# Performance work log

Measured on AMD Instinct MI355X. Metric: run time of the kernel, lower is better.

The kernel has to match this reference:

```python
import jax, jax.numpy as jnp
import numpy as np

PSEUDO3D = True
DO_TUBE = True
DILATION_ITERATIONS = 1

# Neighbor offsets P2..P9 (clockwise from north), as in Zhang-Suen / skimage skeletonize
_OFFS = [(-1, 0), (-1, 1), (0, 1), (1, 1), (1, 0), (1, -1), (0, -1), (-1, -1)]


def _shift(a, dy, dx):
    # out[n, y, x] = a[n, y+dy, x+dx], zero-padded borders (same as skimage's 0-pad)
    N, H, W = a.shape
    p = jnp.pad(a, ((0, 0), (1, 1), (1, 1)))
    return p[:, 1 + dy:1 + dy + H, 1 + dx:1 + dx + W]


def _subiter(img, first):
    # One Zhang-Suen sub-iteration on a stack of 2D slices [N, H, W] (bool)
    P = [_shift(img, dy, dx) for dy, dx in _OFFS]
    B = sum(p.astype(jnp.int32) for p in P)            # nonzero-neighbor count
    seq = P + [P[0]]
    A = sum(((~seq[k]) & seq[k + 1]).astype(jnp.int32) for k in range(8))  # 0->1 transitions
    P2, P3, P4, P5, P6, P7, P8, P9 = P
    if first:
        c = (~(P2 & P4 & P6)) & (~(P4 & P6 & P8))
    else:
        c = (~(P2 & P4 & P8)) & (~(P2 & P6 & P8))
    remove = img & (B >= 2) & (B <= 6) & (A == 1) & c
    return img & ~remove


def _thin_stack(stack):
    # Zhang-Suen thinning of every 2D slice in a [N, H, W] bool stack, run to convergence.
    # All slices are processed in one while_loop; converged slices are fixed points, so
    # extra iterations are no-ops and the result matches per-slice skeletonize.
    def body(state):
        img, _ = state
        new = _subiter(_subiter(img, True), False)
        return new, jnp.any(new != img)

    def cond(state):
        return state[1]

    img, _ = jax.lax.while_loop(cond, body, (stack, jnp.array(True)))
    return img


def _dilate6(v):
    # scipy.ndimage.binary_dilation with the default 6-connected 3D structure, border 0
    D, H, W = v.shape
    p = jnp.pad(v, 1)
    out = v
    for dz, dy, dx in [(1, 0, 0), (-1, 0, 0), (0, 1, 0), (0, -1, 0), (0, 0, 1), (0, 0, -1)]:
        out = out | p[1 + dz:1 + dz + D, 1 + dy:1 + dy + H, 1 + dx:1 + dx + W]
    return out


def setup_inputs() -> dict:
    key = jax.random.key(0)
    gt = jax.random.randint(key, (1, 48, 384, 384), 0, 2).astype(jnp.float32)
    return {"gt_skel": gt}


def reference(gt_skel):
    vol = gt_skel[0]                      # squeeze(axis=0) -> [D, H, W]
    mask = vol == 1.0                     # bool
    skel = _thin_stack(mask)              # per z-slice skeletonize
    if PSEUDO3D:
        # per y-slice: mask[:, y, :] has shape [D, W]
        skel = skel | jnp.transpose(_thin_stack(jnp.transpose(mask, (1, 0, 2))), (1, 0, 2))
        # per x-slice: mask[:, :, x] has shape [D, H]
        skel = skel | jnp.transpose(_thin_stack(jnp.transpose(mask, (2, 0, 1))), (1, 2, 0))
    if DO_TUBE:
        for _ in range(DILATION_ITERATIONS):
            skel = _dilate6(skel)
    skel = skel & mask                    # skel &= gt_skel.astype(bool) (values are 0/1)
    return skel[None].astype(jnp.float32)
```

## Files before the change

kernel.cpp:

```cpp
#include <hip/hip_runtime.h>

typedef unsigned long long u64;

constexpr int D = 48, H = 384, W = 384;
constexpr int WPR = 6;
constexpr int PADW = 8;
constexpr int NVOX = D * H * W;
constexpr int NWVOL = D * H * WPR;
constexpr int MPAD2 = 52;
constexpr int NXY = (D + 2) * PADW;
constexpr int NTILE = D * 36;

constexpr int BAND = 96;
constexpr int HALO = 16;
constexpr int KA = 16;
constexpr int BROWS = BAND + 2 * HALO;
constexpr int NBAND = H / BAND;

__device__ __forceinline__ void fa(u64 a, u64 b, u64 c, u64& s, u64& cy) {
  u64 x = a ^ b;
  s = x ^ c;
  cy = (a & b) | (c & x);
}

__device__ __forceinline__ u64 zs_regs(u64 w00, u64 w01, u64 w02,
                                       u64 w10, u64 w11, u64 w12,
                                       u64 w20, u64 w21, u64 w22, bool first) {
  const u64 P2 = w01;
  const u64 P3 = (w01 >> 1) | (w02 << 63);
  const u64 P4 = (w11 >> 1) | (w12 << 63);
  const u64 P5 = (w21 >> 1) | (w22 << 63);
  const u64 P6 = w21;
  const u64 P7 = (w21 << 1) | (w20 >> 63);
  const u64 P8 = (w11 << 1) | (w10 >> 63);
  const u64 P9 = (w01 << 1) | (w00 >> 63);

  u64 s1, c1, s2, c2, s3, c3, u0, u1, v1, v2;
  fa(P2, P3, P4, s1, c1);
  fa(P5, P6, P7, s2, c2);
  fa(P8, P9, 0ull, s3, c3);
  fa(s1, s2, s3, u0, u1);
  fa(c1, c2, c3, v1, v2);
  u64 b1 = u1 ^ v1, k2 = u1 & v1;
  u64 b2 = v2 ^ k2, b3 = v2 & k2;
  u64 condB = (b1 | b2 | b3) & ~(b3 | (b2 & b1 & u0));

  u64 t0 = ~P2 & P3, t1 = ~P3 & P4, t2 = ~P4 & P5, t3 = ~P5 & P6;
  u64 t4 = ~P6 & P7, t5 = ~P7 & P8, t6 = ~P8 & P9, t7 = ~P9 & P2;
  fa(t0, t1, t2, s1, c1);
  fa(t3, t4, t5, s2, c2);
  fa(t6, t7, 0ull, s3, c3);
  fa(s1, s2, s3, u0, u1);
  fa(c1, c2, c3, v1, v2);
  u64 a1 = u1 ^ v1, j2 = u1 & v1;
  u64 a2 = v2 ^ j2, a3 = v2 & j2;
  u64 condA = u0 & ~(a1 | a2 | a3);

  u64 cc = first ? ((~(P2 & P4 & P6)) & (~(P4 & P6 & P8)))
                 : ((~(P2 & P4 & P8)) & (~(P2 & P6 & P8)));
  return w11 & ~(condB & condA & cc);
}

__device__ __forceinline__ u64 dirty_wave(const u64* __restrict__ U, int mw) {
  const u64 A = U[mw - 1], B = U[mw], C = U[mw + 1], Dw = U[mw + 2];
  const u64 smA = A | (A >> 1 | B << 63) | (A >> 2 | B << 62);
  const u64 smB = B | (B >> 1 | C << 63) | (B >> 2 | C << 62);
  const u64 smC = C | (C >> 1 | Dw << 63) | (C >> 2 | Dw << 62);
  const u64 Dm9 = (smB << 9) | (smA >> 55);
  const u64 Dm1 = (smB << 1) | (smA >> 63);
  const u64 Dp7 = (smB >> 7) | (smC << 57);
  return Dm9 | Dm1 | Dp7;
}

template<int R, bool FIRST>
__device__ __forceinline__ void subpass(const u64* __restrict__ src, u64* __restrict__ dst,
                                        u64* rawW, const u64* rawPrev,
                                        u64* Uw, const u64* Ur,
                                        int* chgflag, int tid) {
  constexpr int NP = (R + 2) * PADW;
  int anych = 0;
  for (int base = 0; base < NP; base += 1024) {
    const int idx = base + tid;
    int changed = 0;
    if (idx < NP) {
      const int mw = 1 + (idx >> 6);
      const u64 dmask = dirty_wave(Ur, mw);
      if ((dmask >> (idx & 63)) & 1ull) {
        const u64 old = src[idx];
        u64 nw = 0;
        if (old) {
          nw = zs_regs(src[idx - PADW - 1], src[idx - PADW], src[idx - PADW + 1],
                       src[idx - 1], old, src[idx + 1],
                       src[idx + PADW - 1], src[idx + PADW], src[idx + PADW + 1], FIRST);
          changed = (nw != old);
        }
        dst[idx] = nw;
        anych |= changed;
      }
    }
    const u64 bal = __ballot(changed != 0);
    if ((tid & 63) == 0 && idx < NP) {
      const int mw = 1 + (idx >> 6);
      rawW[mw] = bal;
      Uw[mw] = bal | rawPrev[mw];
    }
  }
  if (anych) *chgflag = 1;
}

template<int MW>
__device__ __forceinline__ void init_masks(u64 (*raw)[MPAD2], u64 (*Um)[MPAD2], int tid) {
  for (int t = tid; t < 4 * MPAD2; t += 1024) {
    const int arr = t / MPAD2, j = t - arr * MPAD2;
    const u64 v = ((arr & 1) && j >= 1 && j <= MW) ? ~0ull : 0ull;
    if (arr < 2) raw[arr][j] = v; else Um[arr - 2][j] = v;
  }
}

template<bool FIRST>
__device__ __forceinline__ void xy_dense(const u64* __restrict__ src, u64* __restrict__ dst,
                                         int* chgflag, int tid) {
  int anych = 0;
  if (tid < NXY) {
    const u64 old = src[tid];
    u64 nw = 0;
    if (old) {
      nw = zs_regs(src[tid - PADW - 1], src[tid - PADW], src[tid - PADW + 1],
                   src[tid - 1], old, src[tid + 1],
                   src[tid + PADW - 1], src[tid + PADW], src[tid + PADW + 1], FIRST);
      anych = (nw != old);
    }
    dst[tid] = nw;
  }
  if (anych) *chgflag = 1;
}

__device__ __forceinline__ void band_body(const u64* __restrict__ maskP,
                                          u64* __restrict__ curZ,
                                          int zi, int band, u64* Abuf, u64* Bbuf,
                                          u64 (*raw)[MPAD2], u64 (*Um)[MPAD2],
                                          int* s_chg) {
  constexpr int NP = (BROWS + 2) * PADW;
  constexpr int MW = (NP + 63) >> 6;
  const int tid = threadIdx.x;
  const int g0 = band * BAND - HALO;

  for (int idx = tid; idx < NP; idx += 1024) {
    const int rp = idx >> 3, cp = idx & 7;
    const int g = g0 + rp - 1;
    u64 v = 0;
    if (rp >= 1 && rp <= BROWS && cp >= 1 && cp <= 6 && g >= 0 && g < H)
      v = maskP[(zi * H + g) * WPR + (cp - 1)];
    Abuf[idx] = v;
    Bbuf[idx] = 0;
  }
  init_masks<MW>(raw, Um, tid);
  if (tid == 0) s_chg[0] = 0;
  __syncthreads();

  for (int t = 0; t < KA; t += 2) {
    subpass<BROWS, true >(Abuf, Bbuf, raw[0], raw[1], Um[0], Um[1], &s_chg[0], tid);
    __syncthreads();
    subpass<BROWS, false>(Bbuf, Abuf, raw[1], raw[0], Um[1], Um[0], &s_chg[0], tid);
    __syncthreads();
  }

  for (int idx = tid; idx < NP; idx += 1024) {
    const int rp = idx >> 3, cp = idx & 7;
    if (rp < 1 || rp > BROWS || cp < 1 || cp > 6) continue;
    const int g = g0 + rp - 1;
    if (g < band * BAND || g >= band * BAND + BAND) continue;
    curZ[(zi * H + g) * WPR + (cp - 1)] = Abuf[idx];
  }
}

template<int MODE>
__device__ __forceinline__ void thin_xy(const u64* __restrict__ maskP,
                                        u64* __restrict__ dstBuf,
                                        int slice, u64* Abuf, u64* Bbuf,
                                        int* s_chg) {
  const int tid = threadIdx.x;

  if (MODE == 1) {
    if (tid < NXY) {
      const int rp = tid >> 3, cp = tid & 7;
      u64 v = 0;
      if (rp >= 1 && rp <= D && cp >= 1 && cp <= 6)
        v = maskP[((rp - 1) * H + slice) * WPR + (cp - 1)];
      Abuf[tid] = v;
      Bbuf[tid] = 0;
    }
  } else {
    const int lane = tid & 63, wave = tid >> 6;
    const int xw = slice >> 6, xb = slice & 63;
    for (int w = wave; w < NXY; w += 16) {
      const int rp = w >> 3, cp = w & 7;
      u64 val = 0;
      if (rp >= 1 && rp <= D && cp >= 1 && cp <= 6) {
        const int c = (cp - 1) * 64 + lane;
        u64 bit = (maskP[((rp - 1) * H + c) * WPR + xw] >> xb) & 1ull;
        val = __ballot(bit != 0);
      }
      if (lane == 0) { Abuf[w] = val; Bbuf[w] = 0; }
    }
  }
  if (tid < 2) s_chg[tid] = 0;
  __syncthreads();

  int k = 0;
  while (true) {
    xy_dense<true >(Abuf, Bbuf, &s_chg[k], tid);
    __syncthreads();
    if (tid == 0) s_chg[k ^ 1] = 0;
    xy_dense<false>(Bbuf, Abuf, &s_chg[k], tid);
    __syncthreads();
    if (s_chg[k] == 0) break;
    k ^= 1;
  }

  if (tid < NXY) {
    const int rp = tid >> 3, cp = tid & 7;
    if (rp >= 1 && rp <= D && cp >= 1 && cp <= 6) {
      const u64 w = Abuf[tid];
      if (MODE == 1) dstBuf[((rp - 1) * H + slice) * WPR + (cp - 1)] = w;
      else           dstBuf[((rp - 1) * W + slice) * WPR + (cp - 1)] = w;
    }
  }
}

__global__ __launch_bounds__(1024) void thin_bands_xy(const u64* __restrict__ maskP,
                                                      u64* __restrict__ skelY,
                                                      u64* __restrict__ skelX,
                                                      u64* __restrict__ curZ) {
  __shared__ u64 Abuf[(BROWS + 2) * PADW];
  __shared__ u64 Bbuf[(BROWS + 2) * PADW];
  __shared__ u64 raw[2][MPAD2];
  __shared__ u64 Um[2][MPAD2];
  __shared__ int s_chg[2];
  const int b = blockIdx.x;
  if (b < D * NBAND) {
    band_body(maskP, curZ, b >> 2, b & 3, Abuf, Bbuf, raw, Um, s_chg);
  } else {
    const int q = b - D * NBAND;
    if (q < H) thin_xy<1>(maskP, skelY, q, Abuf, Bbuf, s_chg);
    else       thin_xy<2>(maskP, skelX, q - H, Abuf, Bbuf, s_chg);
  }
}

__global__ __launch_bounds__(1024) void thin_z_finish(const u64* __restrict__ curZ,
                                                      u64* __restrict__ skelZ,
                                                      const u64* __restrict__ skelX,
                                                      u64* __restrict__ skelXT) {
  __shared__ u64 Abuf[(H + 2) * PADW];
  __shared__ u64 Bbuf[(H + 2) * PADW];
  __shared__ u64 raw[2][MPAD2];
  __shared__ u64 Um[2][MPAD2];
  __shared__ int s_chg[2];
  const int b = blockIdx.x;
  const int tid = threadIdx.x;

  if (b < D) {
    constexpr int NP = (H + 2) * PADW;
    constexpr int MW = (NP + 63) >> 6;
    for (int idx = tid; idx < NP; idx += 1024) {
      const int rp = idx >> 3, cp = idx & 7;
      u64 v = 0;
      if (rp >= 1 && rp <= H && cp >= 1 && cp <= 6)
        v = curZ[(b * H + (rp - 1)) * WPR + (cp - 1)];
      Abuf[idx] = v;
      Bbuf[idx] = 0;
    }
    init_masks<MW>(raw, Um, tid);
    if (tid < 2) s_chg[tid] = 0;
    __syncthreads();

    int k = 0;
    while (true) {
      subpass<H, true >(Abuf, Bbuf, raw[0], raw[1], Um[0], Um[1], &s_chg[k], tid);
      __syncthreads();
      if (tid == 0) s_chg[k ^ 1] = 0;
      subpass<H, false>(Bbuf, Abuf, raw[1], raw[0], Um[1], Um[0], &s_chg[k], tid);
      __syncthreads();
      if (s_chg[k] == 0) break;
      k ^= 1;
    }

    for (int idx = tid; idx < NP; idx += 1024) {
      const int rp = idx >> 3, cp = idx & 7;
      if (rp < 1 || rp > H || cp < 1 || cp > 6) continue;
      skelZ[(b * H + (rp - 1)) * WPR + (cp - 1)] = Abuf[idx];
    }
  } else {
    const int gw = (b - D) * 16 + (tid >> 6);
    if (gw < NTILE) {
      const int lane = tid & 63;
      const int z = gw / 36, rem = gw - z * 36;
      const int yw = rem / 6, xw = rem - yw * 6;
      const int x = xw * 64 + lane;
      const u64 wx = skelX[(z * W + x) * WPR + yw];
      u64 mine = 0;
      #pragma unroll 8
      for (int j = 0; j < 64; ++j) {
        u64 wj = __ballot((wx >> j) & 1ull);
        if (lane == j) mine = wj;
      }
      const int y = yw * 64 + lane;
      skelXT[(z * H + y) * WPR + xw] = mine;
    }
  }
}

__global__ void init_pack(const float* __restrict__ in, u64* __restrict__ maskP) {
  const int lane = threadIdx.x & 63;
  const int gwave = (blockIdx.x * blockDim.x + threadIdx.x) >> 6;
  const int nwaves = (gridDim.x * blockDim.x) >> 6;
  for (int widx = gwave; widx < NWVOL; widx += nwaves) {
    float v = in[(size_t)widx * 64 + lane];
    u64 w = __ballot(v == 1.0f);
    if (lane == 0) maskP[widx] = w;
  }
}

__global__ __launch_bounds__(256) void dilate_expand(const u64* __restrict__ maskP,
                                                     const u64* __restrict__ sZ,
                                                     const u64* __restrict__ sY,
                                                     const u64* __restrict__ sXT,
                                                     float* __restrict__ out) {
  __shared__ u64 rw[64];
  const int tid = threadIdx.x;
  const int wbase = blockIdx.x * 64;
  if (tid < 64) {
    const int wi = wbase + tid;
    const int wc = wi % WPR;
    const int row = wi / WPR;
    const int y = row % H;
    const int z = row / H;
    const u64 S = sZ[wi] | sY[wi] | sXT[wi];
    const u64 L = (wc > 0) ? (sZ[wi - 1] | sY[wi - 1] | sXT[wi - 1]) : 0ull;
    const u64 Rw = (wc < WPR - 1) ? (sZ[wi + 1] | sY[wi + 1] | sXT[wi + 1]) : 0ull;
    u64 d = S | (S << 1) | (L >> 63) | (S >> 1) | (Rw << 63);
    if (y > 0)     d |= sZ[wi - WPR] | sY[wi - WPR] | sXT[wi - WPR];
    if (y < H - 1) d |= sZ[wi + WPR] | sY[wi + WPR] | sXT[wi + WPR];
    if (z > 0)     d |= sZ[wi - H * WPR] | sY[wi - H * WPR] | sXT[wi - H * WPR];
    if (z < D - 1) d |= sZ[wi + H * WPR] | sY[wi + H * WPR] | sXT[wi + H * WPR];
    rw[tid] = d & maskP[wi];
  }
  __syncthreads();
  float4* o4 = reinterpret_cast<float4*>(out + (size_t)wbase * 64);
  #pragma unroll
  for (int k = 0; k < 4; ++k) {
    const int f = tid + 256 * k;
    const u64 bits = rw[f >> 4] >> ((f & 15) * 4);
    float4 o;
    o.x = (float)(bits & 1ull);
    o.y = (float)((bits >> 1) & 1ull);
    o.z = (float)((bits >> 2) & 1ull);
    o.w = (float)((bits >> 3) & 1ull);
    o4[f] = o;
  }
}

extern "C" void kernel_launch(void* const* d_in, const int* in_sizes, int n_in,
                              void* d_out, int out_size, void* d_ws, size_t ws_size,
                              hipStream_t stream) {
  const float* in = (const float*)d_in[0];
  float* out = (float*)d_out;
  u64* wsw = (u64*)d_ws;
  u64* maskP = wsw;
  u64* skelZ = wsw + NWVOL;
  u64* skelY = wsw + 2 * NWVOL;
  u64* skelX = wsw + 3 * NWVOL;
  u64* skelXT = wsw + 4 * NWVOL;
  u64* curZ = wsw + 5 * NWVOL;

  init_pack<<<1728, 256, 0, stream>>>(in, maskP);
  thin_bands_xy<<<D * NBAND + H + W, 1024, 0, stream>>>(maskP, skelY, skelX, curZ);
  thin_z_finish<<<D + (NTILE + 15) / 16, 1024, 0, stream>>>(curZ, skelZ, skelX, skelXT);
  dilate_expand<<<NWVOL / 64, 256, 0, stream>>>(maskP, skelZ, skelY, skelXT, out);
}
```

Before: 71.47 us.

## Pre-transpose mask for x-slices and shrink thinning blocks to 512 threads

Adds a transpose_in kernel that bit-transposes the packed mask once, so x-slice thinning blocks read contiguous words instead of gathering single bits with per-wave ballots from strided loads. The combined band/xy thinning kernel now launches with 512 threads instead of 1024, since each block only needs about 400–1040 work items; this may allow more blocks per CU. X-slice blocks are also scheduled before y-slice blocks. The cost is an extra kernel launch, one more workspace volume and an extra pass over the packed mask.

Result: faster. 63.97 us (-10.5%).

```diff
diff --git a/kernel.cpp b/kernel.cpp
--- a/kernel.cpp
+++ b/kernel.cpp
@@ -72,14 +72,14 @@
   return Dm9 | Dm1 | Dp7;
 }
 
-template<int R, bool FIRST>
+template<int R, bool FIRST, int NTHR>
 __device__ __forceinline__ void subpass(const u64* __restrict__ src, u64* __restrict__ dst,
                                         u64* rawW, const u64* rawPrev,
                                         u64* Uw, const u64* Ur,
                                         int* chgflag, int tid) {
   constexpr int NP = (R + 2) * PADW;
   int anych = 0;
-  for (int base = 0; base < NP; base += 1024) {
+  for (int base = 0; base < NP; base += NTHR) {
     const int idx = base + tid;
     int changed = 0;
     if (idx < NP) {
@@ -108,9 +108,9 @@
   if (anych) *chgflag = 1;
 }
 
-template<int MW>
+template<int MW, int NTHR>
 __device__ __forceinline__ void init_masks(u64 (*raw)[MPAD2], u64 (*Um)[MPAD2], int tid) {
-  for (int t = tid; t < 4 * MPAD2; t += 1024) {
+  for (int t = tid; t < 4 * MPAD2; t += NTHR) {
     const int arr = t / MPAD2, j = t - arr * MPAD2;
     const u64 v = ((arr & 1) && j >= 1 && j <= MW) ? ~0ull : 0ull;
     if (arr < 2) raw[arr][j] = v; else Um[arr - 2][j] = v;
@@ -145,7 +145,7 @@
   const int tid = threadIdx.x;
   const int g0 = band * BAND - HALO;
 
-  for (int idx = tid; idx < NP; idx += 1024) {
+  for (int idx = tid; idx < NP; idx += 512) {
     const int rp = idx >> 3, cp = idx & 7;
     const int g = g0 + rp - 1;
     u64 v = 0;
@@ -154,18 +154,18 @@
     Abuf[idx] = v;
     Bbuf[idx] = 0;
   }
-  init_masks<MW>(raw, Um, tid);
+  init_masks<MW, 512>(raw, Um, tid);
   if (tid == 0) s_chg[0] = 0;
   __syncthreads();
 
   for (int t = 0; t < KA; t += 2) {
-    subpass<BROWS, true >(Abuf, Bbuf, raw[0], raw[1], Um[0], Um[1], &s_chg[0], tid);
-    __syncthreads();
-    subpass<BROWS, false>(Bbuf, Abuf, raw[1], raw[0], Um[1], Um[0], &s_chg[0], tid);
-    __syncthreads();
-  }
-
-  for (int idx = tid; idx < NP; idx += 1024) {
+    subpass<BROWS, true, 512 >(Abuf, Bbuf, raw[0], raw[1], Um[0], Um[1], &s_chg[0], tid);
+    __syncthreads();
+    subpass<BROWS, false, 512>(Bbuf, Abuf, raw[1], raw[0], Um[1], Um[0], &s_chg[0], tid);
+    __syncthreads();
+  }
+
+  for (int idx = tid; idx < NP; idx += 512) {
     const int rp = idx >> 3, cp = idx & 7;
     if (rp < 1 || rp > BROWS || cp < 1 || cp > 6) continue;
     const int g = g0 + rp - 1;
@@ -175,34 +175,20 @@
 }
 
 template<int MODE>
-__device__ __forceinline__ void thin_xy(const u64* __restrict__ maskP,
+__device__ __forceinline__ void thin_xy(const u64* __restrict__ srcBuf,
                                         u64* __restrict__ dstBuf,
                                         int slice, u64* Abuf, u64* Bbuf,
                                         int* s_chg) {
   const int tid = threadIdx.x;
-
-  if (MODE == 1) {
-    if (tid < NXY) {
-      const int rp = tid >> 3, cp = tid & 7;
-      u64 v = 0;
-      if (rp >= 1 && rp <= D && cp >= 1 && cp <= 6)
-        v = maskP[((rp - 1) * H + slice) * WPR + (cp - 1)];
-      Abuf[tid] = v;
-      Bbuf[tid] = 0;
-    }
-  } else {
-    const int lane = tid & 63, wave = tid >> 6;
-    const int xw = slice >> 6, xb = slice & 63;
-    for (int w = wave; w < NXY; w += 16) {
-      const int rp = w >> 3, cp = w & 7;
-      u64 val = 0;
-      if (rp >= 1 && rp <= D && cp >= 1 && cp <= 6) {
-        const int c = (cp - 1) * 64 + lane;
-        u64 bit = (maskP[((rp - 1) * H + c) * WPR + xw] >> xb) & 1ull;
-        val = __ballot(bit != 0);
-      }
-      if (lane == 0) { Abuf[w] = val; Bbuf[w] = 0; }
-    }
+  constexpr int S = (MODE == 1) ? H : W;
+
+  if (tid < NXY) {
+    const int rp = tid >> 3, cp = tid & 7;
+    u64 v = 0;
+    if (rp >= 1 && rp <= D && cp >= 1 && cp <= 6)
+      v = srcBuf[((rp - 1) * S + slice) * WPR + (cp - 1)];
+    Abuf[tid] = v;
+    Bbuf[tid] = 0;
   }
   if (tid < 2) s_chg[tid] = 0;
   __syncthreads();
@@ -220,18 +206,16 @@
 
   if (tid < NXY) {
     const int rp = tid >> 3, cp = tid & 7;
-    if (rp >= 1 && rp <= D && cp >= 1 && cp <= 6) {
-      const u64 w = Abuf[tid];
-      if (MODE == 1) dstBuf[((rp - 1) * H + slice) * WPR + (cp - 1)] = w;
-      else           dstBuf[((rp - 1) * W + slice) * WPR + (cp - 1)] = w;
-    }
-  }
-}
-
-__global__ __launch_bounds__(1024) void thin_bands_xy(const u64* __restrict__ maskP,
-                                                      u64* __restrict__ skelY,
-                                                      u64* __restrict__ skelX,
-                                                      u64* __restrict__ curZ) {
+    if (rp >= 1 && rp <= D && cp >= 1 && cp <= 6)
+      dstBuf[((rp - 1) * S + slice) * WPR + (cp - 1)] = Abuf[tid];
+  }
+}
+
+__global__ __launch_bounds__(512) void thin_bands_xy(const u64* __restrict__ maskP,
+                                                     const u64* __restrict__ maskPX,
+                                                     u64* __restrict__ skelY,
+                                                     u64* __restrict__ skelX,
+                                                     u64* __restrict__ curZ) {
   __shared__ u64 Abuf[(BROWS + 2) * PADW];
   __shared__ u64 Bbuf[(BROWS + 2) * PADW];
   __shared__ u64 raw[2][MPAD2];
@@ -240,10 +224,10 @@
   const int b = blockIdx.x;
   if (b < D * NBAND) {
     band_body(maskP, curZ, b >> 2, b & 3, Abuf, Bbuf, raw, Um, s_chg);
+  } else if (b < D * NBAND + W) {
+    thin_xy<2>(maskPX, skelX, b - D * NBAND, Abuf, Bbuf, s_chg);
   } else {
-    const int q = b - D * NBAND;
-    if (q < H) thin_xy<1>(maskP, skelY, q, Abuf, Bbuf, s_chg);
-    else       thin_xy<2>(maskP, skelX, q - H, Abuf, Bbuf, s_chg);
+    thin_xy<1>(maskP, skelY, b - D * NBAND - W, Abuf, Bbuf, s_chg);
   }
 }
 
@@ -270,16 +254,16 @@
       Abuf[idx] = v;
       Bbuf[idx] = 0;
     }
-    init_masks<MW>(raw, Um, tid);
+    init_masks<MW, 1024>(raw, Um, tid);
     if (tid < 2) s_chg[tid] = 0;
     __syncthreads();
 
     int k = 0;
     while (true) {
-      subpass<H, true >(Abuf, Bbuf, raw[0], raw[1], Um[0], Um[1], &s_chg[k], tid);
+      subpass<H, true, 1024 >(Abuf, Bbuf, raw[0], raw[1], Um[0], Um[1], &s_chg[k], tid);
       __syncthreads();
       if (tid == 0) s_chg[k ^ 1] = 0;
-      subpass<H, false>(Bbuf, Abuf, raw[1], raw[0], Um[1], Um[0], &s_chg[k], tid);
+      subpass<H, false, 1024>(Bbuf, Abuf, raw[1], raw[0], Um[1], Um[0], &s_chg[k], tid);
       __syncthreads();
       if (s_chg[k] == 0) break;
       k ^= 1;
@@ -319,6 +303,21 @@
     u64 w = __ballot(v == 1.0f);
     if (lane == 0) maskP[widx] = w;
   }
+}
+
+__global__ void transpose_in(const u64* __restrict__ maskP, u64* __restrict__ maskPX) {
+  const int gw = (blockIdx.x * blockDim.x + threadIdx.x) >> 6;
+  const int lane = threadIdx.x & 63;
+  const int z = gw / 36, rem = gw - z * 36;
+  const int yw = rem / 6, xw = rem - yw * 6;
+  const u64 wp = maskP[(z * H + yw * 64 + lane) * WPR + xw];
+  u64 mine = 0;
+  #pragma unroll 8
+  for (int i = 0; i < 64; ++i) {
+    u64 wi = __ballot((wp >> i) & 1ull);
+    if (lane == i) mine = wi;
+  }
+  maskPX[(z * W + xw * 64 + lane) * WPR + yw] = mine;
 }
 
 __global__ __launch_bounds__(256) void dilate_expand(const u64* __restrict__ maskP,
@@ -367,14 +366,16 @@
   float* out = (float*)d_out;
   u64* wsw = (u64*)d_ws;
   u64* maskP = wsw;
-  u64* skelZ = wsw + NWVOL;
-  u64* skelY = wsw + 2 * NWVOL;
-  u64* skelX = wsw + 3 * NWVOL;
-  u64* skelXT = wsw + 4 * NWVOL;
-  u64* curZ = wsw + 5 * NWVOL;
+  u64* maskPX = wsw + NWVOL;
+  u64* skelZ = wsw + 2 * NWVOL;
+  u64* skelY = wsw + 3 * NWVOL;
+  u64* skelX = wsw + 4 * NWVOL;
+  u64* skelXT = wsw + 5 * NWVOL;
+  u64* curZ = wsw + 6 * NWVOL;
 
   init_pack<<<1728, 256, 0, stream>>>(in, maskP);
-  thin_bands_xy<<<D * NBAND + H + W, 1024, 0, stream>>>(maskP, skelY, skelX, curZ);
+  transpose_in<<<(NTILE * 64) / 256, 256, 0, stream>>>(maskP, maskPX);
+  thin_bands_xy<<<D * NBAND + W + H, 512, 0, stream>>>(maskP, maskPX, skelY, skelX, curZ);
   thin_z_finish<<<D + (NTILE + 15) / 16, 1024, 0, stream>>>(curZ, skelZ, skelX, skelXT);
   dilate_expand<<<NWVOL / 64, 256, 0, stream>>>(maskP, skelZ, skelY, skelXT, out);
 }
```
